# Kernel tuning notes

Measured on AMD Instinct MI355X. Metric: run time of the kernel, lower is better.

The kernel has to match this reference:

```python
import jax, jax.numpy as jnp
import numpy as np

B, S, D, H = 2, 2048, 1024, 16
HD = D // H

def setup_inputs() -> dict:
    key = jax.random.key(0)
    ks = jax.random.split(key, 9)
    s = 1.0 / np.sqrt(D)
    return {
        "x": jax.random.normal(ks[0], (B, S, D), jnp.float32),
        "Wq": jax.random.uniform(ks[1], (D, D), jnp.float32, -s, s),
        "bq": jax.random.uniform(ks[2], (D,), jnp.float32, -s, s),
        "Wk": jax.random.uniform(ks[3], (D, D), jnp.float32, -s, s),
        "bk": jax.random.uniform(ks[4], (D,), jnp.float32, -s, s),
        "Wv": jax.random.uniform(ks[5], (D, D), jnp.float32, -s, s),
        "bv": jax.random.uniform(ks[6], (D,), jnp.float32, -s, s),
        "Wo": jax.random.uniform(ks[7], (D, D), jnp.float32, -s, s),
        "bo": jax.random.uniform(ks[8], (D,), jnp.float32, -s, s),
    }

def reference(x, Wq, bq, Wk, bk, Wv, bv, Wo, bo):
    b, s, _ = x.shape
    # projections (torch Linear: y = x @ W.T + b; here W stored as [in,out])
    q = x @ Wq + bq
    k = x @ Wk + bk
    v = x @ Wv + bv
    # [b, h, s, hd]
    q = q.reshape(b, s, H, HD).transpose(0, 2, 1, 3)
    k = k.reshape(b, s, H, HD).transpose(0, 2, 1, 3)
    v = v.reshape(b, s, H, HD).transpose(0, 2, 1, 3)
    scores = jnp.einsum("bhqd,bhkd->bhqk", q, k) / jnp.sqrt(jnp.float32(HD))
    weights = jax.nn.softmax(scores, axis=-1)
    attn = jnp.einsum("bhqk,bhkd->bhqd", weights, v)
    attn = attn.transpose(0, 2, 1, 3).reshape(b, s, D)
    return attn @ Wo + bo
```

## Files before the change

### kernel.cpp

```cpp
#include <hip/hip_runtime.h>
#include <hip/hip_bf16.h>
#include <stdint.h>

#define B_  2
#define S_  2048
#define D_  1024
#define H_  16
#define HD_ 64
#define M_  (B_*S_)

typedef __attribute__((ext_vector_type(8)))  short short8;
typedef __attribute__((ext_vector_type(4)))  float f32x4;
typedef __attribute__((ext_vector_type(16))) float f32x16;

__device__ __forceinline__ unsigned short f2bf(float f) {
  union { float f; unsigned int u; } x; x.f = f;
  unsigned int r = (x.u + 0x7FFFu + ((x.u >> 16) & 1u)) >> 16;
  return (unsigned short)r;
}

__device__ __forceinline__ unsigned int pack2(float a, float b) {
  union { float f; unsigned int u; } x, y; x.f = a; y.f = b;
  return __builtin_amdgcn_perm(y.u + 0x8000u, x.u + 0x8000u, 0x07060302u);
}

typedef const __attribute__((address_space(1))) unsigned int* gas1_t;
typedef __attribute__((address_space(3))) unsigned int* las3_t;

__device__ __forceinline__ void gload_lds16(const void* g, void* l) {
  __builtin_amdgcn_global_load_lds((gas1_t)g, (las3_t)l, 16, 0, 0);
}

__global__ void k_cvt_bf16(const float* __restrict__ x, ushort* __restrict__ o, int n4) {
  int i = blockIdx.x * blockDim.x + threadIdx.x;
  int stride = gridDim.x * blockDim.x;
  for (int j = i; j < n4; j += stride) {
    float4 v = ((const float4*)x)[j];
    ushort4 u = make_ushort4(f2bf(v.x), f2bf(v.y), f2bf(v.z), f2bf(v.w));
    ((ushort4*)o)[j] = u;
  }
}

__global__ void k_transpose_w(const float* __restrict__ w0, const float* __restrict__ w1,
                              const float* __restrict__ w2, const float* __restrict__ w3,
                              ushort* __restrict__ o0, ushort* __restrict__ o1,
                              ushort* __restrict__ o2, ushort* __restrict__ o3) {
  const float* w = (blockIdx.z == 0) ? w0 : (blockIdx.z == 1) ? w1 : (blockIdx.z == 2) ? w2 : w3;
  ushort*      o = (blockIdx.z == 0) ? o0 : (blockIdx.z == 1) ? o1 : (blockIdx.z == 2) ? o2 : o3;
  __shared__ float t[32][33];
  int tx = threadIdx.x & 31, ty = threadIdx.x >> 5;
  int kt = blockIdx.y * 32, nt = blockIdx.x * 32;
  #pragma unroll
  for (int i = 0; i < 4; ++i)
    t[ty + 8 * i][tx] = w[(size_t)(kt + ty + 8 * i) * D_ + nt + tx];
  __syncthreads();
  #pragma unroll
  for (int i = 0; i < 4; ++i)
    o[(size_t)(nt + ty + 8 * i) * D_ + kt + tx] = f2bf(t[tx][ty + 8 * i]);
}

__global__ __launch_bounds__(256) void k_gemm_bt(const ushort* __restrict__ A,
                                                 const ushort* __restrict__ Bt,
                                                 const float* __restrict__ b0,
                                                 const float* __restrict__ b1,
                                                 const float* __restrict__ b2,
                                                 void* __restrict__ o0,
                                                 void* __restrict__ o1,
                                                 void* __restrict__ o2, int mode) {
  __shared__ char smem[2][32768];
  const int tid = threadIdx.x;
  const int w = tid >> 6, lane = tid & 63;
  const int g = lane >> 4, c = lane & 15;
  const int m0 = blockIdx.y * 128, n0 = blockIdx.x * 128;
  const int wm = (w >> 1) * 64, wn = (w & 1) * 64;

  f32x4 acc[4][4];
  #pragma unroll
  for (int i = 0; i < 4; ++i)
    #pragma unroll
    for (int j = 0; j < 4; ++j) acc[i][j] = 0.f;

  const char* Abase = (const char*)A + (size_t)m0 * (D_ * 2);
  const char* Bbase = (const char*)Bt + (size_t)n0 * (D_ * 2);

  auto stage = [&](int buf, int kb) {
    char* ls = &smem[buf][0];
    #pragma unroll
    for (int i = 0; i < 4; ++i) {
      int obase = w * 4096 + i * 1024;
      int ot = obase + lane * 16;
      int u = ot ^ (((ot >> 7) & 7) << 4);
      gload_lds16(Abase + (size_t)(u >> 7) * (D_ * 2) + kb * 128 + (u & 127), ls + obase);
    }
    #pragma unroll
    for (int i = 0; i < 4; ++i) {
      int obase = w * 4096 + i * 1024;
      int ot = obase + lane * 16;
      int u = ot ^ (((ot >> 7) & 7) << 4);
      gload_lds16(Bbase + (size_t)(u >> 7) * (D_ * 2) + kb * 128 + (u & 127), ls + 16384 + obase);
    }
  };

  stage(0, 0);
  int cur = 0;
  for (int kb = 0; kb < D_ / 64; ++kb) {
    __syncthreads();
    if (kb < D_ / 64 - 1) stage(cur ^ 1, kb + 1);
    const char* lsA = &smem[cur][0];
    const char* lsB = lsA + 16384;
    short8 a[4][2], b[4][2];
    #pragma unroll
    for (int f = 0; f < 4; ++f) {
      int rowA = wm + f * 16 + c;
      int rowB = wn + f * 16 + c;
      #pragma unroll
      for (int ks = 0; ks < 2; ++ks) {
        int offA = (rowA * 128 + ks * 64 + g * 16) ^ ((rowA & 7) << 4);
        int offB = (rowB * 128 + ks * 64 + g * 16) ^ ((rowB & 7) << 4);
        a[f][ks] = *(const short8*)(lsA + offA);
        b[f][ks] = *(const short8*)(lsB + offB);
      }
    }
    #pragma unroll
    for (int mf = 0; mf < 4; ++mf)
      #pragma unroll
      for (int nf = 0; nf < 4; ++nf) {
        acc[mf][nf] = __builtin_amdgcn_mfma_f32_16x16x32_bf16(a[mf][0], b[nf][0], acc[mf][nf], 0, 0, 0);
        acc[mf][nf] = __builtin_amdgcn_mfma_f32_16x16x32_bf16(a[mf][1], b[nf][1], acc[mf][nf], 0, 0, 0);
      }
    cur ^= 1;
  }

  const int sec = n0 >> 10;
  const float* bb = (mode == 1) ? b0 : (sec == 0) ? b0 : (sec == 1) ? b1 : b2;
  void* outp = (mode == 1) ? o0 : (sec == 0) ? o0 : (sec == 1) ? o1 : o2;
  #pragma unroll
  for (int nf = 0; nf < 4; ++nf) {
    int col = n0 + wn + nf * 16 + c;
    int lc = col & 1023;
    float bvv = bb[lc];
    #pragma unroll
    for (int mf = 0; mf < 4; ++mf) {
      #pragma unroll
      for (int r = 0; r < 4; ++r) {
        int tok = m0 + wm + mf * 16 + 4 * g + r;
        float v = acc[mf][nf][r] + bvv;
        if (mode == 1) {
          ((float*)outp)[(size_t)tok * D_ + col] = v;
        } else {
          if (sec == 0) v *= 0.18033688011112042f;
          int bi = tok >> 11, si = tok & 2047;
          int h = lc >> 6, hd = lc & 63;
          size_t off = (sec == 2)
            ? ((size_t)(bi * H_ + h) * HD_ + hd) * S_ + si
            : ((size_t)(bi * H_ + h) * S_ + si) * HD_ + hd;
          ((ushort*)outp)[off] = f2bf(v);
        }
      }
    }
  }
}

__global__ __launch_bounds__(256) void k_attn(const ushort* __restrict__ Q,
                                              const ushort* __restrict__ K,
                                              const ushort* __restrict__ Vt,
                                              ushort* __restrict__ O) {
  __shared__ char lds[2][16384];
  const int tid = threadIdx.x;
  const int w = tid >> 6, lane = tid & 63;
  const int ql = lane & 31, hi = lane >> 5;
  const int bid = blockIdx.x;
  const int bh = (bid & 7) * 4 + ((bid >> 3) & 3);
  const int qc = bid >> 5;
  const int q0 = qc * 128 + w * 32;
  const ushort* Qb = Q + (size_t)bh * S_ * HD_;
  const char* Kb2 = (const char*)(K + (size_t)bh * S_ * HD_);
  const char* Vb2 = (const char*)(Vt + (size_t)bh * HD_ * S_);

  short8 qf[4];
  #pragma unroll
  for (int t = 0; t < 4; ++t)
    qf[t] = *(const short8*)(Qb + (size_t)(q0 + ql) * HD_ + 16 * t + 8 * hi);

  auto stageKV = [&](int buf, int k0n) {
    char* ls = &lds[buf][0];
    #pragma unroll
    for (int i = 0; i < 2; ++i) {
      int o = tid * 16 + i * 4096;
      int u = o ^ (((o >> 7) & 7) << 4);
      gload_lds16(Kb2 + (size_t)(k0n + (u >> 7)) * 128 + (u & 127), ls + o);
    }
    #pragma unroll
    for (int i = 0; i < 2; ++i) {
      int o = tid * 16 + i * 4096;
      int u = o ^ (((o >> 7) & 7) << 4);
      gload_lds16(Vb2 + (size_t)(u >> 7) * (S_ * 2) + (size_t)k0n * 2 + (u & 127), ls + 8192 + o);
    }
  };

  f32x16 oacc[2];
  oacc[0] = 0.f; oacc[1] = 0.f;
  float m = -1e30f, l = 0.f;

  stageKV(0, 0);
  int cur = 0;
  for (int k0 = 0; k0 < S_; k0 += 64) {
    __syncthreads();
    if (k0 + 64 < S_) stageKV(cur ^ 1, k0 + 64);
    const char* lsK = &lds[cur][0];
    const char* lsV = lsK + 8192;

    f32x16 st[2];
    #pragma unroll
    for (int n = 0; n < 2; ++n) {
      st[n] = 0.f;
      #pragma unroll
      for (int t = 0; t < 4; ++t) {
        int row = 32 * n + ql, col = 32 * t + 16 * hi;
        short8 kf = *(const short8*)(lsK + ((row * 128 + col) ^ ((row & 7) << 4)));
        st[n] = __builtin_amdgcn_mfma_f32_32x32x16_bf16(kf, qf[t], st[n], 0, 0, 0);
      }
    }

    float red[16];
    #pragma unroll
    for (int i = 0; i < 16; ++i) red[i] = fmaxf(st[0][i], st[1][i]);
    #pragma unroll
    for (int s = 8; s >= 1; s >>= 1)
      #pragma unroll
      for (int i = 0; i < s; ++i) red[i] = fmaxf(red[i], red[i + s]);
    float cmax = fmaxf(red[0], __shfl_xor(red[0], 32));
    float mnew = fmaxf(m, cmax);
    float sc = exp2f(m - mnew);
    m = mnew;
    #pragma unroll
    for (int n = 0; n < 2; ++n)
      #pragma unroll
      for (int i = 0; i < 16; ++i) st[n][i] = exp2f(st[n][i] - mnew);
    #pragma unroll
    for (int i = 0; i < 16; ++i) red[i] = st[0][i] + st[1][i];
    #pragma unroll
    for (int s = 8; s >= 1; s >>= 1)
      #pragma unroll
      for (int i = 0; i < s; ++i) red[i] += red[i + s];
    float ps = red[0] + __shfl_xor(red[0], 32);
    l = l * sc + ps;
    #pragma unroll
    for (int i = 0; i < 16; ++i) { oacc[0][i] *= sc; oacc[1][i] *= sc; }

    short8 pfrag[2][2];
    #pragma unroll
    for (int n = 0; n < 2; ++n) {
      unsigned int pk[4][2];
      #pragma unroll
      for (int b = 0; b < 4; ++b)
        #pragma unroll
        for (int p = 0; p < 2; ++p)
          pk[b][p] = pack2(st[n][4 * b + 2 * p], st[n][4 * b + 2 * p + 1]);
      #pragma unroll
      for (int m2 = 0; m2 < 2; ++m2) {
        union { unsigned int u[4]; short8 v; } fr;
        #pragma unroll
        for (int p = 0; p < 2; ++p) {
          unsigned int xA = (unsigned int)__shfl_xor((int)pk[2 * m2 + 1][p], 32);
          unsigned int xB = (unsigned int)__shfl_xor((int)pk[2 * m2][p], 32);
          fr.u[p]     = hi ? xA : pk[2 * m2][p];
          fr.u[2 + p] = hi ? pk[2 * m2 + 1][p] : xB;
        }
        pfrag[n][m2] = fr.v;
      }
    }

    #pragma unroll
    for (int dt = 0; dt < 2; ++dt)
      #pragma unroll
      for (int n = 0; n < 2; ++n)
        #pragma unroll
        for (int m2 = 0; m2 < 2; ++m2) {
          int row = 32 * dt + ql, col = 64 * n + 32 * m2 + 16 * hi;
          short8 vf = *(const short8*)(lsV + ((row * 128 + col) ^ ((row & 7) << 4)));
          oacc[dt] = __builtin_amdgcn_mfma_f32_32x32x16_bf16(vf, pfrag[n][m2], oacc[dt], 0, 0, 0);
        }
    cur ^= 1;
  }

  const float invl = 1.f / l;
  const int bi = bh >> 4, h = bh & 15;
  const int tok = bi * S_ + q0 + ql;
  #pragma unroll
  for (int dt = 0; dt < 2; ++dt)
    #pragma unroll
    for (int rg = 0; rg < 4; ++rg) {
      ushort4 u;
      u.x = f2bf(oacc[dt][4 * rg + 0] * invl);
      u.y = f2bf(oacc[dt][4 * rg + 1] * invl);
      u.z = f2bf(oacc[dt][4 * rg + 2] * invl);
      u.w = f2bf(oacc[dt][4 * rg + 3] * invl);
      *(ushort4*)(O + (size_t)tok * D_ + h * 64 + dt * 32 + rg * 8 + 4 * hi) = u;
    }
}

extern "C" void kernel_launch(void* const* d_in, const int* in_sizes, int n_in,
                              void* d_out, int out_size, void* d_ws, size_t ws_size,
                              hipStream_t stream) {
  const float* x  = (const float*)d_in[0];
  const float* Wq = (const float*)d_in[1];
  const float* bq = (const float*)d_in[2];
  const float* Wk = (const float*)d_in[3];
  const float* bk = (const float*)d_in[4];
  const float* Wv = (const float*)d_in[5];
  const float* bv = (const float*)d_in[6];
  const float* Wo = (const float*)d_in[7];
  const float* bo = (const float*)d_in[8];
  char* ws = (char*)d_ws;
  const size_t MB = 1024 * 1024;
  ushort* Xbf = (ushort*)(ws + 0);
  ushort* Wt3 = (ushort*)(ws + 8 * MB);
  ushort* Wto = (ushort*)(ws + 14 * MB);
  ushort* Qb  = (ushort*)(ws + 16 * MB);
  ushort* Kb  = (ushort*)(ws + 24 * MB);
  ushort* Vtb = (ushort*)(ws + 32 * MB);
  ushort* Att = (ushort*)(ws + 0);

  k_cvt_bf16<<<1024, 256, 0, stream>>>(x, Xbf, M_ * D_ / 4);
  k_transpose_w<<<dim3(32, 32, 4), 256, 0, stream>>>(
      Wq, Wk, Wv, Wo, Wt3, Wt3 + 1024 * 1024, Wt3 + 2048 * 1024, Wto);
  k_gemm_bt<<<dim3(24, 32), 256, 0, stream>>>(Xbf, Wt3, bq, bk, bv, Qb, Kb, Vtb, 0);
  k_attn<<<512, 256, 0, stream>>>(Qb, Kb, Vtb, Att);
  k_gemm_bt<<<dim3(8, 32), 256, 0, stream>>>(Att, Wto, bo, bo, bo, d_out, d_out, d_out, 1);
}
```

Baseline: 243.8 us.

## Use lazy softmax rescaling, MFMA row sums, and shuffle-free P fragments in attention

The online softmax now rescales the accumulators only when some lane's running max grows by more than 8 (log2 domain). The exponentials are computed directly while packing P to bf16. The row-sum reduction is replaced by an MFMA against a vector of bf16 ones. The cross-lane shuffles that rearranged P fragments are removed by loading V with a matching k-permutation as split 8-byte LDS reads. It also adds a 2-waves-per-EU occupancy hint, and it trades exactness of the max-subtraction for fewer VALU ops, exps and shuffles per tile.

```diff
diff --git a/kernel.cpp b/kernel.cpp
--- a/kernel.cpp
+++ b/kernel.cpp
@@ -161,10 +161,10 @@
   }
 }
 
-__global__ __launch_bounds__(256) void k_attn(const ushort* __restrict__ Q,
-                                              const ushort* __restrict__ K,
-                                              const ushort* __restrict__ Vt,
-                                              ushort* __restrict__ O) {
+__global__ __launch_bounds__(256, 2) void k_attn(const ushort* __restrict__ Q,
+                                                 const ushort* __restrict__ K,
+                                                 const ushort* __restrict__ Vt,
+                                                 ushort* __restrict__ O) {
   __shared__ char lds[2][16384];
   const int tid = threadIdx.x;
   const int w = tid >> 6, lane = tid & 63;
@@ -182,6 +182,10 @@
   for (int t = 0; t < 4; ++t)
     qf[t] = *(const short8*)(Qb + (size_t)(q0 + ql) * HD_ + 16 * t + 8 * hi);
 
+  short8 vones;
+  #pragma unroll
+  for (int i = 0; i < 8; ++i) vones[i] = (short)0x3F80;
+
   auto stageKV = [&](int buf, int k0n) {
     char* ls = &lds[buf][0];
     #pragma unroll
@@ -198,9 +202,9 @@
     }
   };
 
-  f32x16 oacc[2];
-  oacc[0] = 0.f; oacc[1] = 0.f;
-  float m = -1e30f, l = 0.f;
+  f32x16 oacc[2], lacc;
+  oacc[0] = 0.f; oacc[1] = 0.f; lacc = 0.f;
+  float m = -1e30f;
 
   stageKV(0, 0);
   int cur = 0;
@@ -230,23 +234,15 @@
       #pragma unroll
       for (int i = 0; i < s; ++i) red[i] = fmaxf(red[i], red[i + s]);
     float cmax = fmaxf(red[0], __shfl_xor(red[0], 32));
-    float mnew = fmaxf(m, cmax);
-    float sc = exp2f(m - mnew);
-    m = mnew;
-    #pragma unroll
-    for (int n = 0; n < 2; ++n)
-      #pragma unroll
-      for (int i = 0; i < 16; ++i) st[n][i] = exp2f(st[n][i] - mnew);
-    #pragma unroll
-    for (int i = 0; i < 16; ++i) red[i] = st[0][i] + st[1][i];
-    #pragma unroll
-    for (int s = 8; s >= 1; s >>= 1)
-      #pragma unroll
-      for (int i = 0; i < s; ++i) red[i] += red[i + s];
-    float ps = red[0] + __shfl_xor(red[0], 32);
-    l = l * sc + ps;
-    #pragma unroll
-    for (int i = 0; i < 16; ++i) { oacc[0][i] *= sc; oacc[1][i] *= sc; }
+
+    if (!__all(cmax - m <= 8.0f)) {
+      float mnew = fmaxf(m, cmax);
+      float sc = exp2f(m - mnew);
+      m = mnew;
+      #pragma unroll
+      for (int i = 0; i < 16; ++i) { oacc[0][i] *= sc; oacc[1][i] *= sc; }
+      lacc[0] *= sc;
+    }
 
     short8 pfrag[2][2];
     #pragma unroll
@@ -256,35 +252,41 @@
       for (int b = 0; b < 4; ++b)
         #pragma unroll
         for (int p = 0; p < 2; ++p)
-          pk[b][p] = pack2(st[n][4 * b + 2 * p], st[n][4 * b + 2 * p + 1]);
+          pk[b][p] = pack2(exp2f(st[n][4 * b + 2 * p] - m), exp2f(st[n][4 * b + 2 * p + 1] - m));
       #pragma unroll
       for (int m2 = 0; m2 < 2; ++m2) {
         union { unsigned int u[4]; short8 v; } fr;
-        #pragma unroll
-        for (int p = 0; p < 2; ++p) {
-          unsigned int xA = (unsigned int)__shfl_xor((int)pk[2 * m2 + 1][p], 32);
-          unsigned int xB = (unsigned int)__shfl_xor((int)pk[2 * m2][p], 32);
-          fr.u[p]     = hi ? xA : pk[2 * m2][p];
-          fr.u[2 + p] = hi ? pk[2 * m2 + 1][p] : xB;
-        }
+        fr.u[0] = pk[2 * m2][0];     fr.u[1] = pk[2 * m2][1];
+        fr.u[2] = pk[2 * m2 + 1][0]; fr.u[3] = pk[2 * m2 + 1][1];
         pfrag[n][m2] = fr.v;
       }
     }
 
     #pragma unroll
-    for (int dt = 0; dt < 2; ++dt)
+    for (int n = 0; n < 2; ++n)
+      #pragma unroll
+      for (int m2 = 0; m2 < 2; ++m2)
+        lacc = __builtin_amdgcn_mfma_f32_32x32x16_bf16(vones, pfrag[n][m2], lacc, 0, 0, 0);
+
+    #pragma unroll
+    for (int dt = 0; dt < 2; ++dt) {
+      const int rb = (32 * dt + ql) * 128;
+      const int sz = (ql & 7) << 4;
       #pragma unroll
       for (int n = 0; n < 2; ++n)
         #pragma unroll
         for (int m2 = 0; m2 < 2; ++m2) {
-          int row = 32 * dt + ql, col = 64 * n + 32 * m2 + 16 * hi;
-          short8 vf = *(const short8*)(lsV + ((row * 128 + col) ^ ((row & 7) << 4)));
-          oacc[dt] = __builtin_amdgcn_mfma_f32_32x32x16_bf16(vf, pfrag[n][m2], oacc[dt], 0, 0, 0);
+          const int cb = 64 * n + 32 * m2 + 8 * hi;
+          union { struct { unsigned long long a, b; } q; short8 v; } vf;
+          vf.q.a = *(const unsigned long long*)(lsV + ((rb + cb) ^ sz));
+          vf.q.b = *(const unsigned long long*)(lsV + ((rb + cb + 16) ^ sz));
+          oacc[dt] = __builtin_amdgcn_mfma_f32_32x32x16_bf16(vf.v, pfrag[n][m2], oacc[dt], 0, 0, 0);
         }
+    }
     cur ^= 1;
   }
 
-  const float invl = 1.f / l;
+  const float invl = 1.f / lacc[0];
   const int bi = bh >> 4, h = bh & 15;
   const int tok = bi * S_ + q0 + ql;
   #pragma unroll
```

Result: faster. 226.3 us (-7.2%).
